# Kernel optimization log

Hardware: AMD Instinct MI355X
Metric: run time of the kernel (lower is better)

The kernel has to match this reference:

```python
import jax, jax.numpy as jnp
import numpy as np
import itertools, math

# Static config (matches init_kwargs)
DIM = 384
KEY_DIM = 16
NUM_HEADS = 8
ATTN_RATIO = 4
RES = 14
OUT_DIM = 768
RES2 = math.ceil(RES / 2)          # 7
N = RES * RES                      # 196
N2 = RES2 * RES2                   # 49
D = ATTN_RATIO * KEY_DIM           # 64
NH_KD = NUM_HEADS * KEY_DIM        # 128
DH = NUM_HEADS * D                 # 512
SCALE = KEY_DIM ** -0.5
BATCH = 512


def _build_bias_idxs():
    points = list(itertools.product(range(RES), range(RES)))
    points_ = list(itertools.product(range(RES2), range(RES2)))
    ratio = math.ceil(RES / RES2)
    offsets = {}
    idxs = []
    for p1 in points_:
        for p2 in points:
            off = (abs(p1[0] * ratio - p2[0]), abs(p1[1] * ratio - p2[1]))
            if off not in offsets:
                offsets[off] = len(offsets)
            idxs.append(offsets[off])
    return np.array(idxs, dtype=np.int32).reshape(N2, N), len(offsets)


def setup_inputs() -> dict:
    key = jax.random.key(0)
    ks = jax.random.split(key, 16)
    idxs_np, n_off = _build_bias_idxs()
    w = lambda k, shape, s=0.05: (jax.random.normal(k, shape, jnp.float32) * s)
    inp = {
        "x": jax.random.normal(ks[0], (BATCH, DIM, RES, RES), jnp.float32),
        # LGQuery: depthwise 3x3 s2 conv (groups=DIM), then 1x1 conv + BN (folded scale/shift)
        "q_local_w": w(ks[1], (DIM, 1, 3, 3)),
        "q_local_b": w(ks[2], (DIM,)),
        "q_proj_w": w(ks[3], (NH_KD, DIM)),
        "q_proj_b": w(ks[4], (NH_KD,)),
        "q_bn_s": 1.0 + w(ks[5], (NH_KD,)),
        "q_bn_t": w(ks[5], (NH_KD,)),
        # k: 1x1 conv + BN
        "k_w": w(ks[6], (NH_KD, DIM)),
        "k_b": w(ks[7], (NH_KD,)),
        "k_bn_s": 1.0 + w(ks[8], (NH_KD,)),
        "k_bn_t": w(ks[8], (NH_KD,)),
        # v: 1x1 conv + BN
        "v_w": w(ks[9], (DH, DIM)),
        "v_b": w(ks[10], (DH,)),
        "v_bn_s": 1.0 + w(ks[10], (DH,)),
        "v_bn_t": w(ks[10], (DH,)),
        # v_local: depthwise 3x3 s2 (groups=DH) + BN
        "vl_w": w(ks[11], (DH, 1, 3, 3)),
        "vl_b": w(ks[12], (DH,)),
        "vl_bn_s": 1.0 + w(ks[12], (DH,)),
        "vl_bn_t": w(ks[12], (DH,)),
        # proj: GELU -> 1x1 conv -> BN
        "p_w": w(ks[13], (OUT_DIM, DH)),
        "p_b": w(ks[14], (OUT_DIM,)),
        "p_bn_s": 1.0 + w(ks[14], (OUT_DIM,)),
        "p_bn_t": w(ks[14], (OUT_DIM,)),
        # learned relative-position biases + gather indices
        "attn_biases": w(ks[15], (NUM_HEADS, n_off), 0.02),
        "bias_idxs": jnp.asarray(idxs_np),  # [N2, N] int32
    }
    return inp


def _dwconv_s2(x, w, b):
    # depthwise 3x3, stride 2, pad 1, NCHW
    C = x.shape[1]
    y = jax.lax.conv_general_dilated(
        x, w, window_strides=(2, 2), padding=((1, 1), (1, 1)),
        feature_group_count=C, dimension_numbers=("NCHW", "OIHW", "NCHW"))
    return y + b[None, :, None, None]


def _conv1x1_bn(x, w, b, s, t):
    y = jnp.einsum("bchw,oc->bohw", x, w) + b[None, :, None, None]
    return y * s[None, :, None, None] + t[None, :, None, None]


def reference(x, q_local_w, q_local_b, q_proj_w, q_proj_b, q_bn_s, q_bn_t,
              k_w, k_b, k_bn_s, k_bn_t, v_w, v_b, v_bn_s, v_bn_t,
              vl_w, vl_b, vl_bn_s, vl_bn_t, p_w, p_b, p_bn_s, p_bn_t,
              attn_biases, bias_idxs):
    B = x.shape[0]
    # LGQuery: depthwise conv + avgpool(k=1,s=2)==stride subsample, then 1x1+BN
    ql = _dwconv_s2(x, q_local_w, q_local_b) + x[:, :, ::2, ::2]
    q = _conv1x1_bn(ql, q_proj_w, q_proj_b, q_bn_s, q_bn_t)        # [B,128,7,7]
    q = q.reshape(B, NUM_HEADS, KEY_DIM, N2).transpose(0, 1, 3, 2)  # bhqc

    k = _conv1x1_bn(x, k_w, k_b, k_bn_s, k_bn_t).reshape(B, NUM_HEADS, KEY_DIM, N)  # bhck

    v4 = _conv1x1_bn(x, v_w, v_b, v_bn_s, v_bn_t)                   # [B,512,14,14]
    v_local = _dwconv_s2(v4, vl_w, vl_b)
    v_local = v_local * vl_bn_s[None, :, None, None] + vl_bn_t[None, :, None, None]
    v = v4.reshape(B, NUM_HEADS, D, N).transpose(0, 1, 3, 2)        # bhkd

    bias = attn_biases[:, bias_idxs]                                # [H,N2,N]
    attn = jax.nn.softmax(jnp.einsum("bhqc,bhck->bhqk", q, k) * SCALE + bias[None], axis=-1)
    out = jnp.einsum("bhqk,bhkd->bhqd", attn, v)                    # [B,H,N2,D]
    out = out.transpose(0, 1, 3, 2).reshape(B, DH, RES2, RES2) + v_local
    out = jax.nn.gelu(out, approximate=False)                       # torch nn.GELU default (erf)
    out = _conv1x1_bn(out, p_w, p_b, p_bn_s, p_bn_t)                # [B,768,7,7]
    return out
```

## Files before the change

kernel.cpp:

```cpp
#include <hip/hip_runtime.h>
#include <math.h>

#define DIM 384
#define NUM_HEADS 8
#define RES 14
#define RES2 7
#define NPOS 196
#define N2 49
#define DHEAD 64
#define NH_KD 128
#define DH 512
#define OUT_DIM 768
#define BATCH 512
#define SCALE_Q 0.25f

typedef unsigned short u16;
typedef short s16x8 __attribute__((ext_vector_type(8)));
typedef short s16x4 __attribute__((ext_vector_type(4)));
typedef float f32x4 __attribute__((ext_vector_type(4)));
typedef unsigned int u32x2 __attribute__((ext_vector_type(2)));

__device__ __forceinline__ float bf2f(u16 u) {
  union { unsigned int i; float f; } v; v.i = ((unsigned int)u) << 16; return v.f;
}
__device__ __forceinline__ u16 f2bf(float f) {
  union { unsigned int i; float f; } v; v.f = f;
  unsigned int r = v.i + 0x7fffu + ((v.i >> 16) & 1u);
  return (u16)(r >> 16);
}

#define GLD16(gp, lp) __builtin_amdgcn_global_load_lds( \
    (const __attribute__((address_space(1))) void*)(gp), \
    (__attribute__((address_space(3))) void*)(lp), 16, 0, 0)

__global__ __launch_bounds__(256) void k_prep(const float* __restrict__ kw, const float* __restrict__ vw,
                                              const float* __restrict__ qw, const float* __restrict__ pw,
                                              const float* __restrict__ ab, const int* __restrict__ idxs, int noff,
                                              u16* __restrict__ kwb, u16* __restrict__ vwb,
                                              u16* __restrict__ qwb, u16* __restrict__ pwb,
                                              float* __restrict__ bxp) {
  int i = blockIdx.x * 256 + threadIdx.x;
  const int e1 = NH_KD * DIM;
  const int e2 = e1 + DH * DIM;
  const int e3 = e2 + NH_KD * DIM;
  const int e4 = e3 + OUT_DIM * DH;
  const int e5 = e4 + NUM_HEADS * N2 * 256;
  if (i < e1) kwb[i] = f2bf(kw[i]);
  else if (i < e2) vwb[i - e1] = f2bf(vw[i - e1]);
  else if (i < e3) qwb[i - e2] = f2bf(qw[i - e2]);
  else if (i < e4) pwb[i - e3] = f2bf(pw[i - e3]);
  else if (i < e5) {
    int j = i - e4;
    int f = j & 15, c = (j >> 4) & 15;
    int m = (j >> 8) % N2, h = j / (N2 * 256);
    int n = f * 16 + c;
    bxp[j] = (n < NPOS) ? ab[h * noff + idxs[m * NPOS + n]] : 0.f;
  }
}

__global__ __launch_bounds__(256) void k_transpose(const float* __restrict__ x, u16* __restrict__ xt) {
  int b = blockIdx.y, c0 = blockIdx.x * 64;
  __shared__ u16 tile[64][196];
  int tid = threadIdx.x, wave = tid >> 6, lane = tid & 63;
  const float* xb = x + (size_t)b * DIM * NPOS;
  for (int r = wave; r < 64; r += 4) {
    const float* row = xb + (size_t)(c0 + r) * NPOS;
    tile[r][lane]       = f2bf(row[lane]);
    tile[r][lane + 64]  = f2bf(row[lane + 64]);
    tile[r][lane + 128] = f2bf(row[lane + 128]);
    if (lane < 4) tile[r][lane + 192] = f2bf(row[lane + 192]);
  }
  __syncthreads();
  u16* xtb = xt + (size_t)b * NPOS * DIM;
  for (int n = wave; n < NPOS; n += 4)
    xtb[(size_t)n * DIM + c0 + lane] = tile[lane][n];
}

__global__ __launch_bounds__(256) void k_dwconv_q8(const u16* __restrict__ xt, const float* __restrict__ w,
                                                   const float* __restrict__ bias, u16* __restrict__ qlt) {
  int b = blockIdx.y;
  int lid = blockIdx.x * 256 + threadIdx.x;
  if (lid >= N2 * (DIM / 8)) return;
  int n2 = lid / (DIM / 8), c0 = (lid % (DIM / 8)) * 8;
  int r = n2 / RES2, s = n2 % RES2;
  const u16* xb = xt + (size_t)b * NPOS * DIM + c0;

  s16x8 xv[9];
#pragma unroll
  for (int dy = 0; dy < 3; dy++) {
    int ry = 2 * r - 1 + dy;
#pragma unroll
    for (int dx = 0; dx < 3; dx++) {
      int sx = 2 * s - 1 + dx;
      if (ry >= 0 && ry < RES && sx >= 0 && sx < RES)
        xv[dy * 3 + dx] = *(const s16x8*)(xb + (size_t)(ry * RES + sx) * DIM);
      else
        xv[dy * 3 + dx] = (s16x8){0, 0, 0, 0, 0, 0, 0, 0};
    }
  }
  s16x8 resid = *(const s16x8*)(xb + (size_t)(2 * r * RES + 2 * s) * DIM);
  s16x8 o;
#pragma unroll
  for (int e = 0; e < 8; e++) {
    const float* we = w + (size_t)(c0 + e) * 9;
    float a = bias[c0 + e] + bf2f((u16)resid[e]);
#pragma unroll
    for (int t = 0; t < 9; t++) a += we[t] * bf2f((u16)xv[t][e]);
    o[e] = (short)f2bf(a);
  }
  *(s16x8*)(qlt + ((size_t)b * N2 + n2) * DIM + c0) = o;
}

template <int SPLN, bool F32OUT>
__global__ __launch_bounds__(256) void k_gemm_flat(
    const u16* __restrict__ A, const u16* __restrict__ B, void* __restrict__ C,
    const float* __restrict__ cb, const float* __restrict__ bns, const float* __restrict__ bnt,
    int K, int NMT, int ldc, long bstride) {
  __shared__ __align__(16) u16 a_lds[2 * 128 * 32];
  __shared__ __align__(16) u16 b_lds[2 * 128 * 32];
  int nwg = gridDim.x, bx = blockIdx.x;
  int wg = ((nwg & 7) == 0) ? ((bx & 7) * (nwg >> 3) + (bx >> 3)) : bx;
  int mt = wg % NMT, nt = wg / NMT;
  int m0 = mt * 128, n0 = nt * 128;
  int tid = threadIdx.x, w = tid >> 6, l = tid & 63;

  int srow = l >> 2;
  int scol = ((l & 3) ^ ((l >> 3) & 3)) * 8;
  const u16* asrc[2]; const u16* bsrc[2];
#pragma unroll
  for (int c = 0; c < 2; c++) {
    int chunk = w * 2 + c;
    asrc[c] = A + (size_t)(m0 + chunk * 16 + srow) * K + scol;
    bsrc[c] = B + (size_t)(n0 + chunk * 16 + srow) * K + scol;
  }
  char* adst = (char*)a_lds + (w * 2) * 1024 + l * 16;
  char* bdst = (char*)b_lds + (w * 2) * 1024 + l * 16;

  f32x4 acc[4][4];
#pragma unroll
  for (int i = 0; i < 4; i++)
#pragma unroll
    for (int j = 0; j < 4; j++) acc[i][j] = (f32x4){0.f, 0.f, 0.f, 0.f};

  int wm = w >> 1, wn = w & 1;
  int rg8 = ((l >> 4) ^ ((l >> 1) & 3)) * 8;
  int arow = wm * 64 + (l & 15);
  int brow = wn * 64 + (l & 15);

  for (int kk = 0; kk < K; kk += 64) {
#pragma unroll
    for (int c = 0; c < 2; c++) {
      GLD16(asrc[c] + kk,      adst + c * 1024);
      GLD16(asrc[c] + kk + 32, adst + 8192 + c * 1024);
      GLD16(bsrc[c] + kk,      bdst + c * 1024);
      GLD16(bsrc[c] + kk + 32, bdst + 8192 + c * 1024);
    }
    __syncthreads();
#pragma unroll
    for (int hf = 0; hf < 2; hf++) {
      const u16* ah = a_lds + hf * (128 * 32);
      const u16* bh = b_lds + hf * (128 * 32);
      s16x8 af[4], bf[4];
#pragma unroll
      for (int i = 0; i < 4; i++) {
        af[i] = *(const s16x8*)(&ah[(arow + i * 16) * 32 + rg8]);
        bf[i] = *(const s16x8*)(&bh[(brow + i * 16) * 32 + rg8]);
      }
#pragma unroll
      for (int i = 0; i < 4; i++)
#pragma unroll
        for (int j = 0; j < 4; j++)
          acc[i][j] = __builtin_amdgcn_mfma_f32_16x16x32_bf16(af[i], bf[j], acc[i][j], 0, 0, 0);
    }
    __syncthreads();
  }

  int ncol = l & 15, mq = (l >> 4) * 4;
#pragma unroll
  for (int i = 0; i < 4; i++) {
#pragma unroll
    for (int j = 0; j < 4; j++) {
      int n = n0 + wn * 64 + j * 16 + ncol;
#pragma unroll
      for (int r = 0; r < 4; r++) {
        int m = m0 + wm * 64 + i * 16 + mq + r;
        int ch = SPLN ? m : n;
        float val = acc[i][j][r] * bns[ch] + (cb[ch] * bns[ch] + bnt[ch]);
        size_t o;
        if (SPLN) o = (size_t)(n / SPLN) * bstride + (size_t)m * SPLN + (n % SPLN);
        else      o = (size_t)m * ldc + n;
        if (F32OUT) ((float*)C)[o] = val;
        else        ((u16*)C)[o] = f2bf(val);
      }
    }
  }
}

__global__ __launch_bounds__(256) void k_dwconv_v(const u16* __restrict__ v4, const float* __restrict__ w,
    const float* __restrict__ bias, const float* __restrict__ bns, const float* __restrict__ bnt,
    u16* __restrict__ vlt) {
  int b = blockIdx.y, ct = blockIdx.x;
  __shared__ u16 tile[64][196];
  int tid = threadIdx.x, wave = tid >> 6, lane = tid & 63;
  const u16* vbp = v4 + ((size_t)b * DH + ct * 64) * NPOS;
  for (int r = wave; r < 64; r += 4) {
    const u16* row = vbp + (size_t)r * NPOS;
    tile[r][lane]       = row[lane];
    tile[r][lane + 64]  = row[lane + 64];
    tile[r][lane + 128] = row[lane + 128];
    if (lane < 4) tile[r][lane + 192] = row[lane + 192];
  }
  __syncthreads();
  for (int idx = tid; idx < 64 * N2; idx += 256) {
    int cl = idx & 63, n2 = idx >> 6;
    int ch = ct * 64 + cl;
    int r = n2 / RES2, s = n2 % RES2;
    float acc = bias[ch];
#pragma unroll
    for (int dy = 0; dy < 3; dy++) {
      int ry = 2 * r - 1 + dy;
      if (ry < 0 || ry >= RES) continue;
#pragma unroll
      for (int dx = 0; dx < 3; dx++) {
        int sx = 2 * s - 1 + dx;
        if (sx < 0 || sx >= RES) continue;
        acc += w[ch * 9 + dy * 3 + dx] * bf2f(tile[cl][ry * RES + sx]);
      }
    }
    vlt[((size_t)b * N2 + n2) * DH + ch] = f2bf(acc * bns[ch] + bnt[ch]);
  }
}

__global__ __launch_bounds__(256) void k_attn_mfma(const u16* __restrict__ qT, const u16* __restrict__ kT,
    const u16* __restrict__ v4, const float* __restrict__ bxp, const u16* __restrict__ vlT,
    u16* __restrict__ gT) {
  int h = blockIdx.x, b = blockIdx.y;
  __shared__ __align__(16) u16 smem[64 * 32 + 208 * 32 + 64 * 232];
  u16* q_lds = smem;
  u16* k_lds = smem + 64 * 32;
  u16* p_lds = smem + 64 * 32 + 208 * 32;
  float* o_lds = (float*)smem;
  int tid = threadIdx.x, w = tid >> 6, l = tid & 63;

  {
    int row = tid >> 2, part = tid & 3;
    s16x8 val = (s16x8){0, 0, 0, 0, 0, 0, 0, 0};
    if (part < 2 && row < N2)
      val = *(const s16x8*)(qT + ((size_t)b * N2 + row) * NH_KD + h * 16 + part * 8);
    *(s16x8*)(&q_lds[row * 32 + part * 8]) = val;
  }
  for (int row = tid >> 2; row < 208; row += 64) {
    int part = tid & 3;
    s16x8 val = (s16x8){0, 0, 0, 0, 0, 0, 0, 0};
    if (part < 2 && row < NPOS)
      val = *(const s16x8*)(kT + ((size_t)b * NPOS + row) * NH_KD + h * 16 + part * 8);
    *(s16x8*)(&k_lds[row * 32 + part * 8]) = val;
  }
  for (int idx = tid; idx < 64 * 8; idx += 256)
    ((uint*)&p_lds[(idx >> 3) * 232])[104 + (idx & 7)] = 0;

  int mbase = w * 16 + (l >> 4) * 4;
  int ncol = l & 15;
  f32x4 bq[4][4];
#pragma unroll
  for (int r = 0; r < 4; r++) {
    int mm = mbase + r; if (mm > N2 - 1) mm = N2 - 1;
    const float* bb = bxp + (((size_t)h * N2 + mm) * 16 + ncol) * 16;
#pragma unroll
    for (int q = 0; q < 4; q++) bq[r][q] = *(const f32x4*)(bb + q * 4);
  }
  __syncthreads();

  f32x4 s[13];
  {
    s16x8 af = *(const s16x8*)(&q_lds[(w * 16 + (l & 15)) * 32 + (l >> 4) * 8]);
#pragma unroll
    for (int f = 0; f < 13; f++) {
      s16x8 bf = *(const s16x8*)(&k_lds[(f * 16 + (l & 15)) * 32 + (l >> 4) * 8]);
      s[f] = __builtin_amdgcn_mfma_f32_16x16x32_bf16(af, bf, (f32x4){0.f, 0.f, 0.f, 0.f}, 0, 0, 0);
    }
  }

  const u16* vbase = v4 + ((size_t)b * DH + h * DHEAD) * NPOS;
  int vd = l & 15, vq8 = (l >> 4) * 8;
  auto VLOAD = [&](int f, int kk) {
    const u16* p = vbase + (size_t)(f * 16 + vd) * NPOS + kk + vq8;
    s16x8 r;
    ((u32x2*)&r)[0] = *(const u32x2*)(p);
    ((u32x2*)&r)[1] = *(const u32x2*)(p + 4);
    return r;
  };
  s16x8 vb0[4];
#pragma unroll
  for (int f = 0; f < 4; f++) vb0[f] = VLOAD(f, 0);

#pragma unroll
  for (int f = 0; f < 13; f++) {
    int n = f * 16 + ncol;
#pragma unroll
    for (int r = 0; r < 4; r++) {
      int m = mbase + r;
      s[f][r] = (m < N2 && n < NPOS) ? s[f][r] * SCALE_Q + bq[r][f >> 2][f & 3] : -1e30f;
    }
  }
#pragma unroll
  for (int r = 0; r < 4; r++) {
    float mx = s[0][r];
#pragma unroll
    for (int f = 1; f < 13; f++) mx = fmaxf(mx, s[f][r]);
    mx = fmaxf(mx, __shfl_xor(mx, 1)); mx = fmaxf(mx, __shfl_xor(mx, 2));
    mx = fmaxf(mx, __shfl_xor(mx, 4)); mx = fmaxf(mx, __shfl_xor(mx, 8));
    float sum = 0.f;
#pragma unroll
    for (int f = 0; f < 13; f++) { s[f][r] = __expf(s[f][r] - mx); sum += s[f][r]; }
    sum += __shfl_xor(sum, 1); sum += __shfl_xor(sum, 2);
    sum += __shfl_xor(sum, 4); sum += __shfl_xor(sum, 8);
    float inv = 1.f / sum;
#pragma unroll
    for (int f = 0; f < 13; f++) s[f][r] *= inv;
  }
#pragma unroll
  for (int f = 0; f < 13; f++) {
    int n = f * 16 + ncol;
#pragma unroll
    for (int r = 0; r < 4; r++)
      p_lds[(mbase + r) * 232 + n] = f2bf(s[f][r]);
  }
  __syncthreads();

  f32x4 o[4];
#pragma unroll
  for (int f = 0; f < 4; f++) o[f] = (f32x4){0.f, 0.f, 0.f, 0.f};
#pragma unroll
  for (int t = 0; t < 7; t++) {
    int kk = t * 32;
    s16x8 vn[4];
    if (t < 6) {
#pragma unroll
      for (int f = 0; f < 4; f++) vn[f] = VLOAD(f, kk + 32);
    }
    s16x8 pa = *(const s16x8*)(&p_lds[(w * 16 + (l & 15)) * 232 + kk + (l >> 4) * 8]);
#pragma unroll
    for (int f = 0; f < 4; f++)
      o[f] = __builtin_amdgcn_mfma_f32_16x16x32_bf16(pa, vb0[f], o[f], 0, 0, 0);
    if (t < 6) {
#pragma unroll
      for (int f = 0; f < 4; f++) vb0[f] = vn[f];
    }
  }
#pragma unroll
  for (int f = 0; f < 4; f++)
#pragma unroll
    for (int r = 0; r < 4; r++) {
      int m = mbase + r;
      if (m < N2) o_lds[m * 68 + f * 16 + ncol] = o[f][r];
    }
  __syncthreads();

  for (int idx = tid; idx < N2 * 16; idx += 256) {
    int row = idx >> 4, c4 = (idx & 15) << 2;
    f32x4 ov = *(const f32x4*)(&o_lds[row * 68 + c4]);
    size_t go = ((size_t)b * N2 + row) * DH + h * DHEAD + c4;
    s16x4 vv = *(const s16x4*)(vlT + go);
    s16x4 outv;
#pragma unroll
    for (int e = 0; e < 4; e++) {
      float xv = ov[e] + bf2f((u16)vv[e]);
      float g = 0.5f * xv * (1.f + erff(xv * 0.70710678118f));
      outv[e] = (short)f2bf(g);
    }
    *(s16x4*)(gT + go) = outv;
  }
}

extern "C" void kernel_launch(void* const* d_in, const int* in_sizes, int n_in,
                              void* d_out, int out_size, void* d_ws, size_t ws_size,
                              hipStream_t stream) {
  const float* x   = (const float*)d_in[0];
  const float* qlw = (const float*)d_in[1];
  const float* qlb = (const float*)d_in[2];
  const float* qpw = (const float*)d_in[3];
  const float* qpb = (const float*)d_in[4];
  const float* qbs = (const float*)d_in[5];
  const float* qbt = (const float*)d_in[6];
  const float* kw  = (const float*)d_in[7];
  const float* kb  = (const float*)d_in[8];
  const float* kbs = (const float*)d_in[9];
  const float* kbt = (const float*)d_in[10];
  const float* vw  = (const float*)d_in[11];
  const float* vb  = (const float*)d_in[12];
  const float* vbs = (const float*)d_in[13];
  const float* vbt = (const float*)d_in[14];
  const float* vlw = (const float*)d_in[15];
  const float* vlb = (const float*)d_in[16];
  const float* vls = (const float*)d_in[17];
  const float* vlt_in = (const float*)d_in[18];
  const float* pw  = (const float*)d_in[19];
  const float* pb  = (const float*)d_in[20];
  const float* pbs = (const float*)d_in[21];
  const float* pbt = (const float*)d_in[22];
  const float* ab  = (const float*)d_in[23];
  const int*   bidx = (const int*)d_in[24];
  int noff = in_sizes[23] / NUM_HEADS;

  char* ws = (char*)d_ws;
  size_t off = 0;
  auto alloc = [&](size_t bytes) { char* p = ws + off; off += (bytes + 255) & ~(size_t)255; return p; };
  u16* xbT = (u16*)alloc((size_t)BATCH * NPOS * DIM * 2);
  u16* kTm = (u16*)alloc((size_t)BATCH * NPOS * NH_KD * 2);
  u16* qlT = (u16*)alloc((size_t)BATCH * N2 * DIM * 2);
  u16* qTm = (u16*)alloc((size_t)BATCH * N2 * NH_KD * 2);
  u16* v4m = (u16*)alloc((size_t)BATCH * DH * NPOS * 2);
  u16* vlTm = (u16*)alloc((size_t)BATCH * N2 * DH * 2);
  float* bxp = (float*)alloc((size_t)NUM_HEADS * N2 * 16 * 16 * 4);
  u16* kwb = (u16*)alloc((size_t)NH_KD * DIM * 2);
  u16* vwb = (u16*)alloc((size_t)DH * DIM * 2);
  u16* qwb = (u16*)alloc((size_t)NH_KD * DIM * 2);
  u16* pwb = (u16*)alloc((size_t)OUT_DIM * DH * 2);
  u16* gTm = xbT;

  k_prep<<<(888832 + 255) / 256, 256, 0, stream>>>(kw, vw, qpw, pw, ab, bidx, noff,
                                                   kwb, vwb, qwb, pwb, bxp);

  k_transpose<<<dim3(6, BATCH), 256, 0, stream>>>(x, xbT);
  k_dwconv_q8<<<dim3((N2 * (DIM / 8) + 255) / 256, BATCH), 256, 0, stream>>>(xbT, qlw, qlb, qlT);

  k_gemm_flat<0, false><<<784, 256, 0, stream>>>(
      xbT, kwb, kTm, kb, kbs, kbt, DIM, 784, NH_KD, 0);
  k_gemm_flat<NPOS, false><<<3136, 256, 0, stream>>>(
      vwb, xbT, v4m, vb, vbs, vbt, DIM, 4, 0, (long)DH * NPOS);
  k_gemm_flat<0, false><<<196, 256, 0, stream>>>(
      qlT, qwb, qTm, qpb, qbs, qbt, DIM, 196, NH_KD, 0);

  k_dwconv_v<<<dim3(8, BATCH), 256, 0, stream>>>(v4m, vlw, vlb, vls, vlt_in, vlTm);
  k_attn_mfma<<<dim3(NUM_HEADS, BATCH), 256, 0, stream>>>(qTm, kTm, v4m, bxp, vlTm, gTm);

  k_gemm_flat<N2, true><<<1176, 256, 0, stream>>>(
      pwb, gTm, d_out, pb, pbs, pbt, DH, 6, 0, (long)OUT_DIM * N2);
}
```

Baseline: 413.2 us.

## Merge K and V projection GEMMs and stream Q/K directly into attention registers

Concatenates the V and K 1x1 projection weights into a single 640-row weight matrix so that one GEMM launch computes both, with a per-tile epilogue writing K rows into the transposed K buffer. Bias and BN parameters are packed in the prep kernel to match. The attention kernel drops the Q/K LDS staging and loads MFMA operands straight from global memory, loads the bias per quarter to cut register pressure, and raises the occupancy hint to 4 blocks. The merged GEMM's K epilogue writes with a strided, poorly coalesced pattern, and direct global loads in attention rely on cache hits.

```diff
diff --git a/kernel.cpp b/kernel.cpp
--- a/kernel.cpp
+++ b/kernel.cpp
@@ -36,25 +36,31 @@
 __global__ __launch_bounds__(256) void k_prep(const float* __restrict__ kw, const float* __restrict__ vw,
                                               const float* __restrict__ qw, const float* __restrict__ pw,
                                               const float* __restrict__ ab, const int* __restrict__ idxs, int noff,
-                                              u16* __restrict__ kwb, u16* __restrict__ vwb,
-                                              u16* __restrict__ qwb, u16* __restrict__ pwb,
-                                              float* __restrict__ bxp) {
+                                              const float* __restrict__ kb, const float* __restrict__ kbs, const float* __restrict__ kbt,
+                                              const float* __restrict__ vb, const float* __restrict__ vbs, const float* __restrict__ vbt,
+                                              u16* __restrict__ wb, u16* __restrict__ qwb, u16* __restrict__ pwb,
+                                              float* __restrict__ bxp,
+                                              float* __restrict__ cvb, float* __restrict__ cvs, float* __restrict__ cvt) {
   int i = blockIdx.x * 256 + threadIdx.x;
-  const int e1 = NH_KD * DIM;
-  const int e2 = e1 + DH * DIM;
-  const int e3 = e2 + NH_KD * DIM;
-  const int e4 = e3 + OUT_DIM * DH;
-  const int e5 = e4 + NUM_HEADS * N2 * 256;
-  if (i < e1) kwb[i] = f2bf(kw[i]);
-  else if (i < e2) vwb[i - e1] = f2bf(vw[i - e1]);
-  else if (i < e3) qwb[i - e2] = f2bf(qw[i - e2]);
-  else if (i < e4) pwb[i - e3] = f2bf(pw[i - e3]);
-  else if (i < e5) {
-    int j = i - e4;
+  const int E1 = 640 * DIM;
+  const int E2 = E1 + NH_KD * DIM;
+  const int E3 = E2 + OUT_DIM * DH;
+  const int E4 = E3 + NUM_HEADS * N2 * 256;
+  const int E5 = E4 + 3 * 640;
+  if (i < E1) wb[i] = f2bf(i < DH * DIM ? vw[i] : kw[i - DH * DIM]);
+  else if (i < E2) qwb[i - E1] = f2bf(qw[i - E1]);
+  else if (i < E3) pwb[i - E2] = f2bf(pw[i - E2]);
+  else if (i < E4) {
+    int j = i - E3;
     int f = j & 15, c = (j >> 4) & 15;
     int m = (j >> 8) % N2, h = j / (N2 * 256);
     int n = f * 16 + c;
     bxp[j] = (n < NPOS) ? ab[h * noff + idxs[m * NPOS + n]] : 0.f;
+  } else if (i < E5) {
+    int j = i - E4; int c = j % 640, t = j / 640;
+    float v = (c < DH) ? (t == 0 ? vb[c] : t == 1 ? vbs[c] : vbt[c])
+                       : (t == 0 ? kb[c - DH] : t == 1 ? kbs[c - DH] : kbt[c - DH]);
+    (t == 0 ? cvb : t == 1 ? cvs : cvt)[c] = v;
   }
 }
 
@@ -111,9 +117,9 @@
   *(s16x8*)(qlt + ((size_t)b * N2 + n2) * DIM + c0) = o;
 }
 
-template <int SPLN, bool F32OUT>
+template <int SPLN, bool F32OUT, bool KMERGE>
 __global__ __launch_bounds__(256) void k_gemm_flat(
-    const u16* __restrict__ A, const u16* __restrict__ B, void* __restrict__ C,
+    const u16* __restrict__ A, const u16* __restrict__ B, void* __restrict__ C, void* __restrict__ C2,
     const float* __restrict__ cb, const float* __restrict__ bns, const float* __restrict__ bnt,
     int K, int NMT, int ldc, long bstride) {
   __shared__ __align__(16) u16 a_lds[2 * 128 * 32];
@@ -184,13 +190,17 @@
 #pragma unroll
       for (int r = 0; r < 4; r++) {
         int m = m0 + wm * 64 + i * 16 + mq + r;
-        int ch = SPLN ? m : n;
+        int ch = (SPLN || KMERGE) ? m : n;
         float val = acc[i][j][r] * bns[ch] + (cb[ch] * bns[ch] + bnt[ch]);
-        size_t o;
-        if (SPLN) o = (size_t)(n / SPLN) * bstride + (size_t)m * SPLN + (n % SPLN);
-        else      o = (size_t)m * ldc + n;
-        if (F32OUT) ((float*)C)[o] = val;
-        else        ((u16*)C)[o] = f2bf(val);
+        if (KMERGE && m0 >= DH) {
+          ((u16*)C2)[(size_t)n * NH_KD + (m - DH)] = f2bf(val);
+        } else {
+          size_t o;
+          if (SPLN) o = (size_t)(n / SPLN) * bstride + (size_t)m * SPLN + (n % SPLN);
+          else      o = (size_t)m * ldc + n;
+          if (F32OUT) ((float*)C)[o] = val;
+          else        ((u16*)C)[o] = f2bf(val);
+        }
       }
     }
   }
@@ -231,58 +241,36 @@
   }
 }
 
-__global__ __launch_bounds__(256) void k_attn_mfma(const u16* __restrict__ qT, const u16* __restrict__ kT,
+__global__ __launch_bounds__(256, 4) void k_attn_mfma(const u16* __restrict__ qT, const u16* __restrict__ kT,
     const u16* __restrict__ v4, const float* __restrict__ bxp, const u16* __restrict__ vlT,
     u16* __restrict__ gT) {
   int h = blockIdx.x, b = blockIdx.y;
-  __shared__ __align__(16) u16 smem[64 * 32 + 208 * 32 + 64 * 232];
-  u16* q_lds = smem;
-  u16* k_lds = smem + 64 * 32;
-  u16* p_lds = smem + 64 * 32 + 208 * 32;
-  float* o_lds = (float*)smem;
+  __shared__ __align__(16) u16 p_lds[64 * 232];
+  float* o_lds = (float*)p_lds;
   int tid = threadIdx.x, w = tid >> 6, l = tid & 63;
-
-  {
-    int row = tid >> 2, part = tid & 3;
-    s16x8 val = (s16x8){0, 0, 0, 0, 0, 0, 0, 0};
-    if (part < 2 && row < N2)
-      val = *(const s16x8*)(qT + ((size_t)b * N2 + row) * NH_KD + h * 16 + part * 8);
-    *(s16x8*)(&q_lds[row * 32 + part * 8]) = val;
-  }
-  for (int row = tid >> 2; row < 208; row += 64) {
-    int part = tid & 3;
-    s16x8 val = (s16x8){0, 0, 0, 0, 0, 0, 0, 0};
-    if (part < 2 && row < NPOS)
-      val = *(const s16x8*)(kT + ((size_t)b * NPOS + row) * NH_KD + h * 16 + part * 8);
-    *(s16x8*)(&k_lds[row * 32 + part * 8]) = val;
-  }
+  int part = l >> 4, row16 = l & 15;
+  int mbase = w * 16 + part * 4;
+  int ncol = l & 15;
+
   for (int idx = tid; idx < 64 * 8; idx += 256)
     ((uint*)&p_lds[(idx >> 3) * 232])[104 + (idx & 7)] = 0;
 
-  int mbase = w * 16 + (l >> 4) * 4;
-  int ncol = l & 15;
-  f32x4 bq[4][4];
-#pragma unroll
-  for (int r = 0; r < 4; r++) {
-    int mm = mbase + r; if (mm > N2 - 1) mm = N2 - 1;
-    const float* bb = bxp + (((size_t)h * N2 + mm) * 16 + ncol) * 16;
-#pragma unroll
-    for (int q = 0; q < 4; q++) bq[r][q] = *(const f32x4*)(bb + q * 4);
-  }
-  __syncthreads();
-
+  s16x8 af = (s16x8){0, 0, 0, 0, 0, 0, 0, 0};
+  if (part < 2)
+    af = *(const s16x8*)(qT + ((size_t)b * N2 + (w * 16 + row16)) * NH_KD + h * 16 + part * 8);
+
+  const u16* kbase = kT + (size_t)b * NPOS * NH_KD + h * 16 + part * 8;
   f32x4 s[13];
-  {
-    s16x8 af = *(const s16x8*)(&q_lds[(w * 16 + (l & 15)) * 32 + (l >> 4) * 8]);
-#pragma unroll
-    for (int f = 0; f < 13; f++) {
-      s16x8 bf = *(const s16x8*)(&k_lds[(f * 16 + (l & 15)) * 32 + (l >> 4) * 8]);
-      s[f] = __builtin_amdgcn_mfma_f32_16x16x32_bf16(af, bf, (f32x4){0.f, 0.f, 0.f, 0.f}, 0, 0, 0);
-    }
+#pragma unroll
+  for (int f = 0; f < 13; f++) {
+    s16x8 bf = (s16x8){0, 0, 0, 0, 0, 0, 0, 0};
+    if (part < 2)
+      bf = *(const s16x8*)(kbase + (size_t)(f * 16 + row16) * NH_KD);
+    s[f] = __builtin_amdgcn_mfma_f32_16x16x32_bf16(af, bf, (f32x4){0.f, 0.f, 0.f, 0.f}, 0, 0, 0);
   }
 
   const u16* vbase = v4 + ((size_t)b * DH + h * DHEAD) * NPOS;
-  int vd = l & 15, vq8 = (l >> 4) * 8;
+  int vd = l & 15, vq8 = part * 8;
   auto VLOAD = [&](int f, int kk) {
     const u16* p = vbase + (size_t)(f * 16 + vd) * NPOS + kk + vq8;
     s16x8 r;
@@ -295,12 +283,24 @@
   for (int f = 0; f < 4; f++) vb0[f] = VLOAD(f, 0);
 
 #pragma unroll
-  for (int f = 0; f < 13; f++) {
-    int n = f * 16 + ncol;
+  for (int q = 0; q < 4; q++) {
+    f32x4 bqr[4];
 #pragma unroll
     for (int r = 0; r < 4; r++) {
-      int m = mbase + r;
-      s[f][r] = (m < N2 && n < NPOS) ? s[f][r] * SCALE_Q + bq[r][f >> 2][f & 3] : -1e30f;
+      int mm = mbase + r; if (mm > N2 - 1) mm = N2 - 1;
+      bqr[r] = *(const f32x4*)(bxp + (((size_t)h * N2 + mm) * 16 + ncol) * 16 + q * 4);
+    }
+#pragma unroll
+    for (int ff = 0; ff < 4; ff++) {
+      int f = q * 4 + ff;
+      if (f < 13) {
+        int n = f * 16 + ncol;
+#pragma unroll
+        for (int r = 0; r < 4; r++) {
+          int m = mbase + r;
+          s[f][r] = (m < N2 && n < NPOS) ? s[f][r] * SCALE_Q + bqr[r][ff] : -1e30f;
+        }
+      }
     }
   }
 #pragma unroll
@@ -339,7 +339,7 @@
 #pragma unroll
       for (int f = 0; f < 4; f++) vn[f] = VLOAD(f, kk + 32);
     }
-    s16x8 pa = *(const s16x8*)(&p_lds[(w * 16 + (l & 15)) * 232 + kk + (l >> 4) * 8]);
+    s16x8 pa = *(const s16x8*)(&p_lds[(w * 16 + row16) * 232 + kk + part * 8]);
 #pragma unroll
     for (int f = 0; f < 4; f++)
       o[f] = __builtin_amdgcn_mfma_f32_16x16x32_bf16(pa, vb0[f], o[f], 0, 0, 0);
@@ -348,6 +348,8 @@
       for (int f = 0; f < 4; f++) vb0[f] = vn[f];
     }
   }
+  __syncthreads();
+
 #pragma unroll
   for (int f = 0; f < 4; f++)
 #pragma unroll
@@ -413,28 +415,29 @@
   u16* v4m = (u16*)alloc((size_t)BATCH * DH * NPOS * 2);
   u16* vlTm = (u16*)alloc((size_t)BATCH * N2 * DH * 2);
   float* bxp = (float*)alloc((size_t)NUM_HEADS * N2 * 16 * 16 * 4);
-  u16* kwb = (u16*)alloc((size_t)NH_KD * DIM * 2);
-  u16* vwb = (u16*)alloc((size_t)DH * DIM * 2);
+  u16* wb  = (u16*)alloc((size_t)640 * DIM * 2);
   u16* qwb = (u16*)alloc((size_t)NH_KD * DIM * 2);
   u16* pwb = (u16*)alloc((size_t)OUT_DIM * DH * 2);
+  float* cvb = (float*)alloc(640 * 4);
+  float* cvs = (float*)alloc(640 * 4);
+  float* cvt = (float*)alloc(640 * 4);
   u16* gTm = xbT;
 
-  k_prep<<<(888832 + 255) / 256, 256, 0, stream>>>(kw, vw, qpw, pw, ab, bidx, noff,
-                                                   kwb, vwb, qwb, pwb, bxp);
+  k_prep<<<(890752 + 255) / 256, 256, 0, stream>>>(kw, vw, qpw, pw, ab, bidx, noff,
+                                                   kb, kbs, kbt, vb, vbs, vbt,
+                                                   wb, qwb, pwb, bxp, cvb, cvs, cvt);
 
   k_transpose<<<dim3(6, BATCH), 256, 0, stream>>>(x, xbT);
   k_dwconv_q8<<<dim3((N2 * (DIM / 8) + 255) / 256, BATCH), 256, 0, stream>>>(xbT, qlw, qlb, qlT);
 
-  k_gemm_flat<0, false><<<784, 256, 0, stream>>>(
-      xbT, kwb, kTm, kb, kbs, kbt, DIM, 784, NH_KD, 0);
-  k_gemm_flat<NPOS, false><<<3136, 256, 0, stream>>>(
-      vwb, xbT, v4m, vb, vbs, vbt, DIM, 4, 0, (long)DH * NPOS);
-  k_gemm_flat<0, false><<<196, 256, 0, stream>>>(
-      qlT, qwb, qTm, qpb, qbs, qbt, DIM, 196, NH_KD, 0);
+  k_gemm_flat<NPOS, false, true><<<3920, 256, 0, stream>>>(
+      wb, xbT, v4m, kTm, cvb, cvs, cvt, DIM, 5, 0, (long)DH * NPOS);
+  k_gemm_flat<0, false, false><<<196, 256, 0, stream>>>(
+      qlT, qwb, qTm, nullptr, qpb, qbs, qbt, DIM, 196, NH_KD, 0);
 
   k_dwconv_v<<<dim3(8, BATCH), 256, 0, stream>>>(v4m, vlw, vlb, vls, vlt_in, vlTm);
   k_attn_mfma<<<dim3(NUM_HEADS, BATCH), 256, 0, stream>>>(qTm, kTm, v4m, bxp, vlTm, gTm);
 
-  k_gemm_flat<N2, true><<<1176, 256, 0, stream>>>(
-      pwb, gTm, d_out, pb, pbs, pbt, DH, 6, 0, (long)OUT_DIM * N2);
-}
+  k_gemm_flat<N2, true, false><<<1176, 256, 0, stream>>>(
+      pwb, gTm, d_out, nullptr, pb, pbs, pbt, DH, 6, 0, (long)OUT_DIM * N2);
+}
```

Result: no change. 418.4 us (+1.2%).
